# Kernel optimization log

Hardware: AMD Instinct MI355X
Metric: run time of the kernel (lower is better)

## Reference

```python
import jax, jax.numpy as jnp
import numpy as np

NUM_HEADS = 16
ROPE_BASE = 10000.0

def rotate_half(x):
    h = x.shape[-1] // 2
    return jnp.concatenate([-x[..., h:], x[..., :h]], axis=-1)

def setup_inputs() -> dict:
    key = jax.random.key(0)
    k1, k2, k3, k4 = jax.random.split(key, 4)
    B, T, H = 2, 2048, 1024
    hidden_state = jax.random.normal(k1, (B, T, H), dtype=jnp.float32)
    # right-padding mask: per-batch valid lengths
    lengths = jnp.array([2048, 1536], dtype=jnp.int32)
    attention_mask = (jnp.arange(T, dtype=jnp.int32)[None, :] < lengths[:, None]).astype(jnp.int32)
    s = 1.0 / np.sqrt(H)
    w_qkv = jax.random.normal(k2, (H, 3 * H), dtype=jnp.float32) * s
    b_qkv = jax.random.normal(k3, (3 * H,), dtype=jnp.float32) * 0.01
    w_out = jax.random.normal(k4, (H, H), dtype=jnp.float32) * s
    return {"hidden_state": hidden_state, "attention_mask": attention_mask,
            "w_qkv": w_qkv, "b_qkv": b_qkv, "w_out": w_out}

def reference(hidden_state, attention_mask, w_qkv, b_qkv, w_out):
    B, T, H = hidden_state.shape
    hd = H // NUM_HEADS
    qkv = hidden_state @ w_qkv + b_qkv                      # [B,T,3H]
    qkv = qkv.reshape(B, T, NUM_HEADS, 3 * hd).swapaxes(1, 2)  # [B,h,T,3d]
    q, k, v = qkv[..., :hd], qkv[..., hd:2 * hd], qkv[..., 2 * hd:]
    # rotary embedding (cache computed in fp32, as in torch module)
    inv_freq = 1.0 / (ROPE_BASE ** (jnp.arange(0, hd, 2, dtype=jnp.float32) / hd))
    t = jnp.arange(T, dtype=jnp.float32)
    freqs = jnp.outer(t, inv_freq)                          # [T, hd/2]
    emb = jnp.concatenate([freqs, freqs], axis=-1)          # [T, hd]
    cos = jnp.cos(emb)[None, None]                          # [1,1,T,hd]
    sin = jnp.sin(emb)[None, None]
    q = q * cos + rotate_half(q) * sin
    k = k * cos + rotate_half(k) * sin
    scale = 1.0 / jnp.sqrt(jnp.asarray(hd, dtype=q.dtype))
    scores = jnp.einsum('bhqd,bhkd->bhqk', q, k) * scale    # [B,h,T,T]
    causal = jnp.triu(jnp.ones((T, T), dtype=bool), k=1)    # True = masked (future)
    pad = (attention_mask == 0)[:, None, None, :]           # True = masked (padded key)
    mask = causal[None, None] | pad
    scores = jnp.where(mask, jnp.finfo(scores.dtype).min, scores)
    attn = jax.nn.softmax(scores, axis=-1)
    out = jnp.einsum('bhqk,bhkd->bhqd', attn, v)            # [B,h,T,d]
    out = out.swapaxes(1, 2).reshape(B, T, H)
    return out @ w_out
```

## Files before the change

### kernel.cpp

```cpp
#include <hip/hip_runtime.h>
#include <math.h>

typedef __attribute__((ext_vector_type(8))) short short8;
typedef __attribute__((ext_vector_type(4))) short short4v;
typedef __attribute__((ext_vector_type(4))) float floatx4;

#define T_SEQ 2048
#define NHEADS 16
#define HID 1024

#if __has_builtin(__builtin_amdgcn_mfma_f32_16x16x16bf16_1k)
#define MFMA16(a,b,c) __builtin_amdgcn_mfma_f32_16x16x16bf16_1k(a,b,c,0,0,0)
#elif __has_builtin(__builtin_amdgcn_mfma_f32_16x16x16_bf16)
#define MFMA16(a,b,c) __builtin_amdgcn_mfma_f32_16x16x16_bf16(a,b,c,0,0,0)
#else
#define MFMA16(a,b,c) (c)
#endif

#if __has_builtin(__builtin_amdgcn_exp2f)
#define EXP2F(x) __builtin_amdgcn_exp2f(x)
#else
#define EXP2F(x) exp2f(x)
#endif

__device__ __forceinline__ ushort f2b(float x){
  union { float f; unsigned u; } c; c.f = x;
  unsigned r = c.u + 0x7fffu + ((c.u >> 16) & 1u);
  return (ushort)(r >> 16);
}

__device__ __forceinline__ floatx4 fzero4(){
  floatx4 v; v[0]=0.f; v[1]=0.f; v[2]=0.f; v[3]=0.f; return v;
}

__device__ __forceinline__ void gl_lds16(const ushort* g, ushort* l){
  __builtin_amdgcn_global_load_lds(
      (const __attribute__((address_space(1))) void*)g,
      (__attribute__((address_space(3))) void*)l, 16, 0, 0);
}


__global__ __launch_bounds__(256) void prep(
    const float* __restrict__ hidden, const float* __restrict__ w_qkv,
    const float* __restrict__ w_out, const int* __restrict__ amask,
    ushort* __restrict__ hO, ushort* __restrict__ wqkvT, ushort* __restrict__ woutT,
    float2* __restrict__ cs, int* __restrict__ Lb)
{
  __shared__ __align__(16) char smem[32 * 33 * 4];
  int blk = blockIdx.x;
  int tid = threadIdx.x;

  if (blk < 4096){
    int i = blk * 256 + tid;
    float4 v = ((const float4*)hidden)[i];
    ushort4 o;
    o.x = f2b(v.x); o.y = f2b(v.y); o.z = f2b(v.z); o.w = f2b(v.w);
    ((ushort4*)hO)[i] = o;
  } else if (blk < 8192){
    const float* in; ushort* out; int R, C, bx, by;
    if (blk < 7168){
      int t = blk - 4096; bx = t % 96; by = t / 96;
      in = w_qkv; out = wqkvT; R = 1024; C = 3072;
    } else {
      int t = blk - 7168; bx = t & 31; by = t >> 5;
      in = w_out; out = woutT; R = 1024; C = 1024;
    }
    float (*tile)[33] = (float(*)[33])smem;
    int c0 = bx * 32, r0 = by * 32;
    int tx = tid & 31, ty = tid >> 5;
    #pragma unroll
    for (int i = 0; i < 4; i++){
      int r = ty + i * 8;
      tile[r][tx] = in[(size_t)(r0 + r) * C + c0 + tx];
    }
    __syncthreads();
    #pragma unroll
    for (int i = 0; i < 4; i++){
      int r = ty + i * 8;
      out[(size_t)(c0 + r) * R + r0 + tx] = f2b(tile[tx][r]);
    }
  } else if (blk < 8448){
    int idx = (blk - 8192) * 256 + tid;
    int t = idx >> 5, i = idx & 31;
    float invf = powf(10000.0f, -(float)i / 32.0f);
    float a = (float)t * invf;
    cs[idx] = make_float2(cosf(a), sinf(a));
  } else {
    int b = blk - 8448;
    int* red = (int*)smem;
    int s = 0;
    for (int i = tid; i < T_SEQ; i += 256) s += amask[b * T_SEQ + i];
    red[tid] = s; __syncthreads();
    for (int o = 128; o > 0; o >>= 1){
      if (tid < o) red[tid] += red[tid + o];
      __syncthreads();
    }
    if (tid == 0) Lb[b] = red[0];
  }
}


__global__ __launch_bounds__(256) void gemm_qkv(
    const ushort* __restrict__ A, const ushort* __restrict__ Bt,
    const float* __restrict__ bias,
    ushort* __restrict__ qO, ushort* __restrict__ kO, ushort* __restrict__ vT,
    const float2* __restrict__ cs)
{
  __shared__ __align__(16) ushort As[2][4096];
  __shared__ __align__(16) ushort Bs[2][4096];
  int tid = threadIdx.x;
  int bm = blockIdx.x, bn = blockIdx.y;
  int wave = tid >> 6, lane = tid & 63;
  int wm = wave >> 1, wn = wave & 1;
  int quad = lane >> 4, l15 = lane & 15;

  int srow0 = wave * 32 + (lane >> 2);
  int scol  = (lane & 3) * 8;
  const ushort* baseA = &A[(size_t)(bm * 128 + srow0) * 1024 + scol];
  const ushort* baseB = &Bt[(size_t)(bn * 128 + srow0) * 1024 + scol];

  floatx4 acc[4][4];
  for (int i = 0; i < 4; i++) for (int j = 0; j < 4; j++) acc[i][j] = fzero4();

  gl_lds16(baseA,             &As[0][wave * 1024]);
  gl_lds16(baseA + 16 * 1024, &As[0][wave * 1024 + 512]);
  gl_lds16(baseB,             &Bs[0][wave * 1024]);
  gl_lds16(baseB + 16 * 1024, &Bs[0][wave * 1024 + 512]);
  __syncthreads();

  for (int kt = 0; kt < 32; ++kt){
    int cur = kt & 1;
    if (kt < 31){
      const ushort* gA = baseA + (kt + 1) * 32;
      const ushort* gB = baseB + (kt + 1) * 32;
      gl_lds16(gA,             &As[cur ^ 1][wave * 1024]);
      gl_lds16(gA + 16 * 1024, &As[cur ^ 1][wave * 1024 + 512]);
      gl_lds16(gB,             &Bs[cur ^ 1][wave * 1024]);
      gl_lds16(gB + 16 * 1024, &Bs[cur ^ 1][wave * 1024 + 512]);
    }
    short8 af[4], bfr[4];
    #pragma unroll
    for (int i = 0; i < 4; i++) af[i]  = *(const short8*)&As[cur][(wm * 64 + i * 16 + l15) * 32 + quad * 8];
    #pragma unroll
    for (int i = 0; i < 4; i++) bfr[i] = *(const short8*)&Bs[cur][(wn * 64 + i * 16 + l15) * 32 + quad * 8];
    #pragma unroll
    for (int mt = 0; mt < 4; mt++)
      #pragma unroll
      for (int nt = 0; nt < 4; nt++)
        acc[mt][nt] = __builtin_amdgcn_mfma_f32_16x16x32_bf16(af[mt], bfr[nt], acc[mt][nt], 0, 0, 0);
    __syncthreads();
  }

  int g = bn * 2 + wn;
  int h = g / 3, comp = g - h * 3;

  if (comp == 2){
    #pragma unroll
    for (int nt = 0; nt < 4; nt++){
      int d = nt * 16 + l15;
      float bv = bias[g * 64 + d];
      #pragma unroll
      for (int mt = 0; mt < 4; mt++){
        int row = bm * 128 + wm * 64 + mt * 16 + quad * 4;
        int t = row & (T_SEQ - 1), b_ = row >> 11;
        ushort4 o;
        o.x = f2b(acc[mt][nt][0] + bv);
        o.y = f2b(acc[mt][nt][1] + bv);
        o.z = f2b(acc[mt][nt][2] + bv);
        o.w = f2b(acc[mt][nt][3] + bv);
        *(ushort4*)&vT[(size_t)((b_ * NHEADS + h) * 64 + d) * T_SEQ + t] = o;
      }
    }
  } else {
    ushort* outP = (comp == 0) ? qO : kO;
    float qs = (comp == 0) ? 0.125f * 1.44269504089f : 1.0f;
    float bv[4], bp[4];
    #pragma unroll
    for (int nt = 0; nt < 4; nt++){
      bv[nt] = bias[g * 64 + nt * 16 + l15];
      bp[nt] = bias[g * 64 + ((nt * 16 + l15) ^ 32)];
    }
    #pragma unroll
    for (int mt = 0; mt < 4; mt++)
      #pragma unroll
      for (int r = 0; r < 4; r++){
        int row = bm * 128 + wm * 64 + mt * 16 + quad * 4 + r;
        int t = row & (T_SEQ - 1), b_ = row >> 11;
        float2 c0 = cs[t * 32 + l15];
        float2 c1 = cs[t * 32 + 16 + l15];
        size_t base = (size_t)((b_ * NHEADS + h) * T_SEQ + t) * 64 + l15;
        #pragma unroll
        for (int nt = 0; nt < 4; nt++){
          float cvv = (nt & 1) ? c1.x : c0.x;
          float svv = (nt & 1) ? c1.y : c0.y;
          float sgn = (nt < 2) ? -1.0f : 1.0f;
          float val = acc[mt][nt][r] + bv[nt];
          float pv  = acc[mt][nt ^ 2][r] + bp[nt];
          outP[base + nt * 16] = f2b((val * cvv + sgn * pv * svv) * qs);
        }
      }
  }
}


__global__ __launch_bounds__(256) void attn(
    const ushort* __restrict__ qB, const ushort* __restrict__ kB,
    const ushort* __restrict__ vTB, const int* __restrict__ Lb,
    ushort* __restrict__ oB)
{
  __shared__ __align__(16) ushort SH[2][8192];
  int tid = threadIdx.x;
  int bh = blockIdx.x;
  int qt = 31 - blockIdx.y;
  int b = bh >> 4, h = bh & 15;
  int wave = tid >> 6, lane = tid & 63;
  int quad = lane >> 4, l15 = lane & 15;
  int q0 = qt * 64;
  int L = Lb[b];

  const ushort* Qb  = qB + (size_t)bh * T_SEQ * 64;
  const ushort* Kb  = kB + (size_t)bh * T_SEQ * 64;
  const ushort* VtB = vTB + (size_t)bh * 64 * T_SEQ;

  int qrow = q0 + wave * 16 + l15;
  short8 qf0 = *(const short8*)&Qb[(size_t)qrow * 64 + quad * 8];
  short8 qf1 = *(const short8*)&Qb[(size_t)qrow * 64 + 32 + quad * 8];

  int lr = lane >> 3, ch = lane & 7;
  int sw = (ch ^ lr) * 8;
  int l7 = l15 & 7;

  float l_i = 0.f;
  floatx4 oacc[4];
  #pragma unroll
  for (int nt = 0; nt < 4; nt++) oacc[nt] = fzero4();

  int lastkb = qt;
  int lkb2 = (L - 1) >> 6;
  if (lkb2 < lastkb) lastkb = lkb2;

  auto stageKV = [&](int kb, int buf){
    int k0 = kb * 64;
    const ushort* gK = &Kb[(size_t)(k0 + wave * 16 + lr) * 64 + sw];
    gl_lds16(gK,          &SH[buf][(wave * 16) * 64]);
    gl_lds16(gK + 8 * 64, &SH[buf][(wave * 16 + 8) * 64]);
    const ushort* gV = &VtB[(size_t)(wave * 16 + lr) * T_SEQ + k0 + sw];
    gl_lds16(gV,             &SH[buf][4096 + (wave * 16) * 64]);
    gl_lds16(gV + 8 * T_SEQ, &SH[buf][4096 + (wave * 16 + 8) * 64]);
  };

  stageKV(0, 0);
  __syncthreads();

  for (int kb = 0; kb <= lastkb; ++kb){
    int cur = kb & 1;
    if (kb < lastkb) stageKV(kb + 1, cur ^ 1);
    const ushort* Ks = &SH[cur][0];
    const ushort* Vt = &SH[cur][4096];
    int k0 = kb * 64;

    floatx4 sacc[4];
    #pragma unroll
    for (int e = 0; e < 4; e++){
      short8 kf0 = *(const short8*)&Ks[(e * 16 + l15) * 64 + ((quad ^ l7) * 8)];
      short8 kf1 = *(const short8*)&Ks[(e * 16 + l15) * 64 + (((quad | 4) ^ l7) * 8)];
      floatx4 z = fzero4();
      z = __builtin_amdgcn_mfma_f32_16x16x32_bf16(kf0, qf0, z, 0, 0, 0);
      z = __builtin_amdgcn_mfma_f32_16x16x32_bf16(kf1, qf1, z, 0, 0, 0);
      sacc[e] = z;
    }

    float p[4][4];
    bool needm = (kb == qt) || (k0 + 64 > L);
    if (needm){
      #pragma unroll
      for (int e = 0; e < 4; e++)
        #pragma unroll
        for (int r = 0; r < 4; r++){
          int key = k0 + e * 16 + quad * 4 + r;
          float ev = EXP2F(sacc[e][r]);
          p[e][r] = (key <= qrow && key < L) ? ev : 0.f;
        }
    } else {
      #pragma unroll
      for (int e = 0; e < 4; e++)
        #pragma unroll
        for (int r = 0; r < 4; r++) p[e][r] = EXP2F(sacc[e][r]);
    }
    float s0 = 0.f, s1 = 0.f, s2 = 0.f, s3 = 0.f;
    #pragma unroll
    for (int e = 0; e < 4; e++){
      s0 += p[e][0]; s1 += p[e][1]; s2 += p[e][2]; s3 += p[e][3];
    }
    l_i += (s0 + s1) + (s2 + s3);

    short4v pf[4];
    #pragma unroll
    for (int e = 0; e < 4; e++){
      union { unsigned u[2]; short4v v; } pk;
      pk.u[0] = (__float_as_uint(p[e][1]) & 0xffff0000u) | (__float_as_uint(p[e][0]) >> 16);
      pk.u[1] = (__float_as_uint(p[e][3]) & 0xffff0000u) | (__float_as_uint(p[e][2]) >> 16);
      pf[e] = pk.v;
    }

    #pragma unroll
    for (int nt = 0; nt < 4; nt++){
      #pragma unroll
      for (int e = 0; e < 4; e++){
        int cw = e * 2 + (quad >> 1);
        short4v vf = *(const short4v*)&Vt[(nt * 16 + l15) * 64 + ((cw ^ l7) * 8) + (quad & 1) * 4];
        oacc[nt] = MFMA16(vf, pf[e], oacc[nt]);
      }
    }
    __syncthreads();
  }

  l_i += __shfl_xor(l_i, 16);
  l_i += __shfl_xor(l_i, 32);
  float inv = 1.f / l_i;

  ushort (*Ot)[80] = (ushort(*)[80])&SH[0][0];
  #pragma unroll
  for (int nt = 0; nt < 4; nt++){
    ushort4 o;
    o.x = f2b(oacc[nt][0] * inv);
    o.y = f2b(oacc[nt][1] * inv);
    o.z = f2b(oacc[nt][2] * inv);
    o.w = f2b(oacc[nt][3] * inv);
    *(ushort4*)&Ot[wave * 16 + l15][nt * 16 + quad * 4] = o;
  }
  __syncthreads();
  int r = tid >> 2, c = (tid & 3) * 16;
  short8 o0 = *(const short8*)&Ot[r][c];
  short8 o1 = *(const short8*)&Ot[r][c + 8];
  ushort* dst = &oB[(size_t)((b * T_SEQ + q0 + r) * NHEADS + h) * 64 + c];
  *(short8*)dst = o0;
  *(short8*)(dst + 8) = o1;
}


__global__ __launch_bounds__(256) void gemm_out_k(
    const ushort* __restrict__ A, const ushort* __restrict__ Bt,
    float* __restrict__ out)
{
  __shared__ __align__(16) ushort As[2][4096];
  __shared__ __align__(16) ushort Bs[2][2048];
  int tid = threadIdx.x;
  int bm = blockIdx.x, bn = blockIdx.y;
  int wave = tid >> 6, lane = tid & 63;
  int wm = wave >> 1, wn = wave & 1;
  int quad = lane >> 4, l15 = lane & 15;

  int lr4 = lane >> 2;
  int sc  = (lane & 3) * 8;
  const ushort* baseA = &A[(size_t)(bm * 128 + wave * 32 + lr4) * 1024 + sc];
  const ushort* baseB = &Bt[(size_t)(bn * 64 + wave * 16 + lr4) * 1024 + sc];

  floatx4 acc[4][2];
  for (int i = 0; i < 4; i++) for (int j = 0; j < 2; j++) acc[i][j] = fzero4();

  gl_lds16(baseA,             &As[0][wave * 1024]);
  gl_lds16(baseA + 16 * 1024, &As[0][wave * 1024 + 512]);
  gl_lds16(baseB,             &Bs[0][wave * 512]);
  __syncthreads();

  for (int kt = 0; kt < 32; ++kt){
    int cur = kt & 1;
    if (kt < 31){
      const ushort* gA = baseA + (kt + 1) * 32;
      const ushort* gB = baseB + (kt + 1) * 32;
      gl_lds16(gA,             &As[cur ^ 1][wave * 1024]);
      gl_lds16(gA + 16 * 1024, &As[cur ^ 1][wave * 1024 + 512]);
      gl_lds16(gB,             &Bs[cur ^ 1][wave * 512]);
    }
    short8 af[4], bfr[2];
    #pragma unroll
    for (int i = 0; i < 4; i++) af[i]  = *(const short8*)&As[cur][(wm * 64 + i * 16 + l15) * 32 + quad * 8];
    #pragma unroll
    for (int j = 0; j < 2; j++) bfr[j] = *(const short8*)&Bs[cur][(wn * 32 + j * 16 + l15) * 32 + quad * 8];
    #pragma unroll
    for (int mt = 0; mt < 4; mt++)
      #pragma unroll
      for (int nt = 0; nt < 2; nt++)
        acc[mt][nt] = __builtin_amdgcn_mfma_f32_16x16x32_bf16(af[mt], bfr[nt], acc[mt][nt], 0, 0, 0);
    __syncthreads();
  }

  #pragma unroll
  for (int nt = 0; nt < 2; nt++){
    int n = bn * 64 + wn * 32 + nt * 16 + l15;
    #pragma unroll
    for (int mt = 0; mt < 4; mt++)
      #pragma unroll
      for (int r = 0; r < 4; r++){
        int row = bm * 128 + wm * 64 + mt * 16 + quad * 4 + r;
        out[(size_t)row * 1024 + n] = acc[mt][nt][r];
      }
  }
}


extern "C" void kernel_launch(void* const* d_in, const int* in_sizes, int n_in,
                              void* d_out, int out_size, void* d_ws, size_t ws_size,
                              hipStream_t stream)
{
  const float* hidden = (const float*)d_in[0];
  const int*   amask  = (const int*)d_in[1];
  const float* w_qkv  = (const float*)d_in[2];
  const float* b_qkv  = (const float*)d_in[3];
  const float* w_out  = (const float*)d_in[4];
  float* out = (float*)d_out;

  char* ws = (char*)d_ws;
  ushort* hO    = (ushort*)(ws);
  ushort* wqkvT = (ushort*)(ws + 8388608);
  ushort* woutT = (ushort*)(ws + 14680064);
  ushort* qB    = (ushort*)(ws + 16777216);
  ushort* kB    = (ushort*)(ws + 25165824);
  ushort* vT    = (ushort*)(ws + 33554432);
  float2* cs    = (float2*)(ws + 41943040);
  int*    Lb    = (int*)(ws + 42467328);

  prep<<<8450, 256, 0, stream>>>(hidden, w_qkv, w_out, amask, hO, wqkvT, woutT, cs, Lb);
  gemm_qkv<<<dim3(32, 24), 256, 0, stream>>>(hO, wqkvT, b_qkv, qB, kB, vT, cs);
  attn<<<dim3(32, 32), 256, 0, stream>>>(qB, kB, vT, Lb, hO );
  gemm_out_k<<<dim3(32, 16), 256, 0, stream>>>(hO, woutT, out);
}
```

Baseline: 179.5 us.

## Restructure QKV GEMM to 256x256 tiles with swizzled LDS and staged pipeline

The QKV projection GEMM moves from 128x128 tiles with 4 waves to 256x256 tiles with 8 waves and a K-step of 64. It XOR-swizzles the LDS layout to avoid bank conflicts and remaps block IDs so neighbouring blocks share operand tiles in cache. It also splits each K-step into four MFMA phases, interleaving global-to-LDS prefetch with barriers and s_setprio. The aim is more operand reuse per byte loaded and better overlap of loads with MFMA, at the cost of only 192 blocks and higher register and LDS use (128KB of LDS per block).

```diff
diff --git a/kernel.cpp b/kernel.cpp
--- a/kernel.cpp
+++ b/kernel.cpp
@@ -100,58 +100,133 @@
 }
 
 
-__global__ __launch_bounds__(256) void gemm_qkv(
+__global__ __launch_bounds__(512, 2) void gemm_qkv(
     const ushort* __restrict__ A, const ushort* __restrict__ Bt,
     const float* __restrict__ bias,
     ushort* __restrict__ qO, ushort* __restrict__ kO, ushort* __restrict__ vT,
     const float2* __restrict__ cs)
 {
-  __shared__ __align__(16) ushort As[2][4096];
-  __shared__ __align__(16) ushort Bs[2][4096];
+  __shared__ __align__(16) ushort As[2][16384];
+  __shared__ __align__(16) ushort Bs[2][16384];
   int tid = threadIdx.x;
-  int bm = blockIdx.x, bn = blockIdx.y;
+  int bid = blockIdx.x;
+  int swz = (bid & 7) * 24 + (bid >> 3);
+  int bm = swz / 12, bn = swz - bm * 12;
   int wave = tid >> 6, lane = tid & 63;
-  int wm = wave >> 1, wn = wave & 1;
-  int quad = lane >> 4, l15 = lane & 15;
-
-  int srow0 = wave * 32 + (lane >> 2);
-  int scol  = (lane & 3) * 8;
-  const ushort* baseA = &A[(size_t)(bm * 128 + srow0) * 1024 + scol];
-  const ushort* baseB = &Bt[(size_t)(bn * 128 + srow0) * 1024 + scol];
-
-  floatx4 acc[4][4];
-  for (int i = 0; i < 4; i++) for (int j = 0; j < 4; j++) acc[i][j] = fzero4();
-
-  gl_lds16(baseA,             &As[0][wave * 1024]);
-  gl_lds16(baseA + 16 * 1024, &As[0][wave * 1024 + 512]);
-  gl_lds16(baseB,             &Bs[0][wave * 1024]);
-  gl_lds16(baseB + 16 * 1024, &Bs[0][wave * 1024 + 512]);
-  __syncthreads();
-
-  for (int kt = 0; kt < 32; ++kt){
+  int wm = wave >> 2, wn = wave & 3;
+  int quad = lane >> 4, l15 = lane & 15, l7 = lane & 7;
+
+  int srow = tid >> 3, sslot = tid & 7;
+  const ushort* gA = A  + (size_t)(bm * 256 + srow) * 1024 + ((sslot ^ (srow & 7)) << 3);
+  const ushort* gB = Bt + (size_t)(bn * 256 + srow) * 1024 + ((sslot ^ (srow & 7)) << 3);
+
+  auto stageA = [&](int buf, int kt){
+    #pragma unroll
+    for (int i = 0; i < 4; i++)
+      gl_lds16(gA + (size_t)i * 64 * 1024 + kt * 64, &As[buf][i * 4096 + wave * 512]);
+  };
+  auto stageB = [&](int buf, int kt){
+    #pragma unroll
+    for (int i = 0; i < 4; i++)
+      gl_lds16(gB + (size_t)i * 64 * 1024 + kt * 64, &Bs[buf][i * 4096 + wave * 512]);
+  };
+
+  int s0 = ((quad)     ^ l7) << 3;
+  int s1 = ((quad + 4) ^ l7) << 3;
+
+  floatx4 acc[8][4];
+  #pragma unroll
+  for (int i = 0; i < 8; i++)
+    #pragma unroll
+    for (int j = 0; j < 4; j++) acc[i][j] = fzero4();
+
+  stageA(0, 0); stageB(0, 0);
+  asm volatile("s_waitcnt vmcnt(0)" ::: "memory");
+  __builtin_amdgcn_s_barrier();
+
+  short8 af[4][2], bfr[4][2];
+
+  for (int kt = 0; kt < 16; ++kt){
     int cur = kt & 1;
-    if (kt < 31){
-      const ushort* gA = baseA + (kt + 1) * 32;
-      const ushort* gB = baseB + (kt + 1) * 32;
-      gl_lds16(gA,             &As[cur ^ 1][wave * 1024]);
-      gl_lds16(gA + 16 * 1024, &As[cur ^ 1][wave * 1024 + 512]);
-      gl_lds16(gB,             &Bs[cur ^ 1][wave * 1024]);
-      gl_lds16(gB + 16 * 1024, &Bs[cur ^ 1][wave * 1024 + 512]);
-    }
-    short8 af[4], bfr[4];
-    #pragma unroll
-    for (int i = 0; i < 4; i++) af[i]  = *(const short8*)&As[cur][(wm * 64 + i * 16 + l15) * 32 + quad * 8];
-    #pragma unroll
-    for (int i = 0; i < 4; i++) bfr[i] = *(const short8*)&Bs[cur][(wn * 64 + i * 16 + l15) * 32 + quad * 8];
+    const ushort* Ac = &As[cur][0];
+    const ushort* Bc = &Bs[cur][0];
+
+    #pragma unroll
+    for (int mt = 0; mt < 4; mt++){
+      int ro = (wm * 128 + mt * 16 + l15) * 64;
+      af[mt][0] = *(const short8*)&Ac[ro + s0];
+      af[mt][1] = *(const short8*)&Ac[ro + s1];
+    }
+    #pragma unroll
+    for (int nt = 0; nt < 2; nt++){
+      int ro = (wn * 64 + nt * 16 + l15) * 64;
+      bfr[nt][0] = *(const short8*)&Bc[ro + s0];
+      bfr[nt][1] = *(const short8*)&Bc[ro + s1];
+    }
+    if (kt < 15) stageA(cur ^ 1, kt + 1);
+    __builtin_amdgcn_s_barrier();
+    __builtin_amdgcn_s_setprio(1);
     #pragma unroll
     for (int mt = 0; mt < 4; mt++)
       #pragma unroll
-      for (int nt = 0; nt < 4; nt++)
-        acc[mt][nt] = __builtin_amdgcn_mfma_f32_16x16x32_bf16(af[mt], bfr[nt], acc[mt][nt], 0, 0, 0);
-    __syncthreads();
-  }
-
-  int g = bn * 2 + wn;
+      for (int nt = 0; nt < 2; nt++){
+        acc[mt][nt] = __builtin_amdgcn_mfma_f32_16x16x32_bf16(af[mt][0], bfr[nt][0], acc[mt][nt], 0, 0, 0);
+        acc[mt][nt] = __builtin_amdgcn_mfma_f32_16x16x32_bf16(af[mt][1], bfr[nt][1], acc[mt][nt], 0, 0, 0);
+      }
+    __builtin_amdgcn_s_setprio(0);
+    __builtin_amdgcn_s_barrier();
+
+    #pragma unroll
+    for (int nt = 2; nt < 4; nt++){
+      int ro = (wn * 64 + nt * 16 + l15) * 64;
+      bfr[nt][0] = *(const short8*)&Bc[ro + s0];
+      bfr[nt][1] = *(const short8*)&Bc[ro + s1];
+    }
+    if (kt < 15) stageB(cur ^ 1, kt + 1);
+    __builtin_amdgcn_s_barrier();
+    __builtin_amdgcn_s_setprio(1);
+    #pragma unroll
+    for (int mt = 0; mt < 4; mt++)
+      #pragma unroll
+      for (int nt = 2; nt < 4; nt++){
+        acc[mt][nt] = __builtin_amdgcn_mfma_f32_16x16x32_bf16(af[mt][0], bfr[nt][0], acc[mt][nt], 0, 0, 0);
+        acc[mt][nt] = __builtin_amdgcn_mfma_f32_16x16x32_bf16(af[mt][1], bfr[nt][1], acc[mt][nt], 0, 0, 0);
+      }
+    __builtin_amdgcn_s_setprio(0);
+    __builtin_amdgcn_s_barrier();
+
+    #pragma unroll
+    for (int mt = 0; mt < 4; mt++){
+      int ro = (wm * 128 + 64 + mt * 16 + l15) * 64;
+      af[mt][0] = *(const short8*)&Ac[ro + s0];
+      af[mt][1] = *(const short8*)&Ac[ro + s1];
+    }
+    __builtin_amdgcn_s_barrier();
+    __builtin_amdgcn_s_setprio(1);
+    #pragma unroll
+    for (int mt = 0; mt < 4; mt++)
+      #pragma unroll
+      for (int nt = 0; nt < 2; nt++){
+        acc[4 + mt][nt] = __builtin_amdgcn_mfma_f32_16x16x32_bf16(af[mt][0], bfr[nt][0], acc[4 + mt][nt], 0, 0, 0);
+        acc[4 + mt][nt] = __builtin_amdgcn_mfma_f32_16x16x32_bf16(af[mt][1], bfr[nt][1], acc[4 + mt][nt], 0, 0, 0);
+      }
+    __builtin_amdgcn_s_setprio(0);
+    __builtin_amdgcn_s_barrier();
+
+    __builtin_amdgcn_s_setprio(1);
+    #pragma unroll
+    for (int mt = 0; mt < 4; mt++)
+      #pragma unroll
+      for (int nt = 2; nt < 4; nt++){
+        acc[4 + mt][nt] = __builtin_amdgcn_mfma_f32_16x16x32_bf16(af[mt][0], bfr[nt][0], acc[4 + mt][nt], 0, 0, 0);
+        acc[4 + mt][nt] = __builtin_amdgcn_mfma_f32_16x16x32_bf16(af[mt][1], bfr[nt][1], acc[4 + mt][nt], 0, 0, 0);
+      }
+    __builtin_amdgcn_s_setprio(0);
+    if (kt < 15) asm volatile("s_waitcnt vmcnt(0)" ::: "memory");
+    __builtin_amdgcn_s_barrier();
+  }
+
+  int g = bn * 4 + wn;
   int h = g / 3, comp = g - h * 3;
 
   if (comp == 2){
@@ -160,8 +235,8 @@
       int d = nt * 16 + l15;
       float bv = bias[g * 64 + d];
       #pragma unroll
-      for (int mt = 0; mt < 4; mt++){
-        int row = bm * 128 + wm * 64 + mt * 16 + quad * 4;
+      for (int mt = 0; mt < 8; mt++){
+        int row = bm * 256 + wm * 128 + mt * 16 + quad * 4;
         int t = row & (T_SEQ - 1), b_ = row >> 11;
         ushort4 o;
         o.x = f2b(acc[mt][nt][0] + bv);
@@ -181,10 +256,10 @@
       bp[nt] = bias[g * 64 + ((nt * 16 + l15) ^ 32)];
     }
     #pragma unroll
-    for (int mt = 0; mt < 4; mt++)
+    for (int mt = 0; mt < 8; mt++)
       #pragma unroll
       for (int r = 0; r < 4; r++){
-        int row = bm * 128 + wm * 64 + mt * 16 + quad * 4 + r;
+        int row = bm * 256 + wm * 128 + mt * 16 + quad * 4 + r;
         int t = row & (T_SEQ - 1), b_ = row >> 11;
         float2 c0 = cs[t * 32 + l15];
         float2 c1 = cs[t * 32 + 16 + l15];
@@ -422,7 +497,7 @@
   int*    Lb    = (int*)(ws + 42467328);
 
   prep<<<8450, 256, 0, stream>>>(hidden, w_qkv, w_out, amask, hO, wqkvT, woutT, cs, Lb);
-  gemm_qkv<<<dim3(32, 24), 256, 0, stream>>>(hO, wqkvT, b_qkv, qB, kB, vT, cs);
+  gemm_qkv<<<dim3(192), 512, 0, stream>>>(hO, wqkvT, b_qkv, qB, kB, vT, cs);
   attn<<<dim3(32, 32), 256, 0, stream>>>(qB, kB, vT, Lb, hO );
   gemm_out_k<<<dim3(32, 16), 256, 0, stream>>>(hO, woutT, out);
 }
```

Result: no change. 179.3 us (-0.2%).

## Enlarge QKV GEMM tile to 256x256 with 8 waves and swizzled LDS

Applied to the files above, without the earlier changes.

The QKV projection GEMM now uses 256x256 output tiles computed by 8 waves (512 threads), with a 64-wide K step split into two halves. It adds an XOR swizzle on LDS columns to avoid bank conflicts, a block-index remap for L2 locality, explicit vmcnt waits with raw barriers, and interleaves the next tile's loads with MFMA groups under raised wave priority. The goal is more reuse per loaded byte and better overlap of global-to-LDS traffic with matrix math. In exchange it uses far more LDS and registers per block, and launches only 192 blocks, which may underfill the GPU.

```diff
diff --git a/kernel.cpp b/kernel.cpp
--- a/kernel.cpp
+++ b/kernel.cpp
@@ -100,58 +100,91 @@
 }
 
 
-__global__ __launch_bounds__(256) void gemm_qkv(
+__global__ __launch_bounds__(512, 2) void gemm_qkv(
     const ushort* __restrict__ A, const ushort* __restrict__ Bt,
     const float* __restrict__ bias,
     ushort* __restrict__ qO, ushort* __restrict__ kO, ushort* __restrict__ vT,
     const float2* __restrict__ cs)
 {
-  __shared__ __align__(16) ushort As[2][4096];
-  __shared__ __align__(16) ushort Bs[2][4096];
+  __shared__ __align__(16) ushort As[2][16384];
+  __shared__ __align__(16) ushort Bs[2][16384];
   int tid = threadIdx.x;
-  int bm = blockIdx.x, bn = blockIdx.y;
+  int bid = blockIdx.x;
+  int swz = (bid & 7) * 24 + (bid >> 3);
+  int bm = swz / 12, bn = swz - bm * 12;
   int wave = tid >> 6, lane = tid & 63;
-  int wm = wave >> 1, wn = wave & 1;
+  int wm = wave >> 2, wn = wave & 3;
   int quad = lane >> 4, l15 = lane & 15;
 
-  int srow0 = wave * 32 + (lane >> 2);
-  int scol  = (lane & 3) * 8;
-  const ushort* baseA = &A[(size_t)(bm * 128 + srow0) * 1024 + scol];
-  const ushort* baseB = &Bt[(size_t)(bn * 128 + srow0) * 1024 + scol];
-
-  floatx4 acc[4][4];
-  for (int i = 0; i < 4; i++) for (int j = 0; j < 4; j++) acc[i][j] = fzero4();
-
-  gl_lds16(baseA,             &As[0][wave * 1024]);
-  gl_lds16(baseA + 16 * 1024, &As[0][wave * 1024 + 512]);
-  gl_lds16(baseB,             &Bs[0][wave * 1024]);
-  gl_lds16(baseB + 16 * 1024, &Bs[0][wave * 1024 + 512]);
-  __syncthreads();
-
-  for (int kt = 0; kt < 32; ++kt){
-    int cur = kt & 1;
-    if (kt < 31){
-      const ushort* gA = baseA + (kt + 1) * 32;
-      const ushort* gB = baseB + (kt + 1) * 32;
-      gl_lds16(gA,             &As[cur ^ 1][wave * 1024]);
-      gl_lds16(gA + 16 * 1024, &As[cur ^ 1][wave * 1024 + 512]);
-      gl_lds16(gB,             &Bs[cur ^ 1][wave * 1024]);
-      gl_lds16(gB + 16 * 1024, &Bs[cur ^ 1][wave * 1024 + 512]);
-    }
-    short8 af[4], bfr[4];
-    #pragma unroll
-    for (int i = 0; i < 4; i++) af[i]  = *(const short8*)&As[cur][(wm * 64 + i * 16 + l15) * 32 + quad * 8];
-    #pragma unroll
-    for (int i = 0; i < 4; i++) bfr[i] = *(const short8*)&Bs[cur][(wn * 64 + i * 16 + l15) * 32 + quad * 8];
-    #pragma unroll
-    for (int mt = 0; mt < 4; mt++)
-      #pragma unroll
-      for (int nt = 0; nt < 4; nt++)
-        acc[mt][nt] = __builtin_amdgcn_mfma_f32_16x16x32_bf16(af[mt], bfr[nt], acc[mt][nt], 0, 0, 0);
-    __syncthreads();
-  }
-
-  int g = bn * 2 + wn;
+  int srow = tid >> 2;
+  int sg = (lane & 3) ^ ((lane >> 3) & 3);
+  const ushort* gA = A  + (size_t)(bm * 256 + srow) * 1024 + sg * 8;
+  const ushort* gB = Bt + (size_t)(bn * 256 + srow) * 1024 + sg * 8;
+
+  auto stageU = [&](const ushort* g, ushort* Lbase, int kh, int kt2){
+    #pragma unroll
+    for (int i = 0; i < 2; i++)
+      gl_lds16(g + (size_t)(i * 128) * 1024 + kt2 * 64 + kh * 32,
+               Lbase + kh * 8192 + (i * 128 + wave * 16) * 32);
+  };
+
+  int sA = (quad ^ ((l15 >> 1) & 3)) * 8;
+
+  floatx4 acc[8][4];
+  #pragma unroll
+  for (int i = 0; i < 8; i++)
+    #pragma unroll
+    for (int j = 0; j < 4; j++) acc[i][j] = fzero4();
+
+  stageU(gA, &As[0][0], 0, 0);
+  stageU(gB, &Bs[0][0], 0, 0);
+  stageU(gA, &As[0][0], 1, 0);
+  stageU(gB, &Bs[0][0], 1, 0);
+
+  for (int kt = 0; kt < 16; ++kt){
+    int cur = kt & 1, nxt = cur ^ 1;
+    const ushort* Ac = &As[cur][0];
+    const ushort* Bc = &Bs[cur][0];
+
+    #pragma unroll
+    for (int kh = 0; kh < 2; kh++){
+      if (kh == 0 || kt < 15) asm volatile("s_waitcnt vmcnt(4)" ::: "memory");
+      else                    asm volatile("s_waitcnt vmcnt(0)" ::: "memory");
+      __builtin_amdgcn_s_barrier();
+
+      short8 af[8], bfr[4];
+      #pragma unroll
+      for (int mt = 0; mt < 8; mt++)
+        af[mt] = *(const short8*)&Ac[kh * 8192 + (wm * 128 + mt * 16 + l15) * 32 + sA];
+      #pragma unroll
+      for (int nt = 0; nt < 2; nt++)
+        bfr[nt] = *(const short8*)&Bc[kh * 8192 + (wn * 64 + nt * 16 + l15) * 32 + sA];
+      if (kt < 15) stageU(gA, &As[nxt][0], kh, kt + 1);
+
+      __builtin_amdgcn_s_setprio(1);
+      #pragma unroll
+      for (int mt = 0; mt < 8; mt++)
+        #pragma unroll
+        for (int nt = 0; nt < 2; nt++)
+          acc[mt][nt] = __builtin_amdgcn_mfma_f32_16x16x32_bf16(af[mt], bfr[nt], acc[mt][nt], 0, 0, 0);
+      __builtin_amdgcn_s_setprio(0);
+
+      #pragma unroll
+      for (int nt = 2; nt < 4; nt++)
+        bfr[nt] = *(const short8*)&Bc[kh * 8192 + (wn * 64 + nt * 16 + l15) * 32 + sA];
+      if (kt < 15) stageU(gB, &Bs[nxt][0], kh, kt + 1);
+
+      __builtin_amdgcn_s_setprio(1);
+      #pragma unroll
+      for (int mt = 0; mt < 8; mt++)
+        #pragma unroll
+        for (int nt = 2; nt < 4; nt++)
+          acc[mt][nt] = __builtin_amdgcn_mfma_f32_16x16x32_bf16(af[mt], bfr[nt], acc[mt][nt], 0, 0, 0);
+      __builtin_amdgcn_s_setprio(0);
+    }
+  }
+
+  int g = bn * 4 + wn;
   int h = g / 3, comp = g - h * 3;
 
   if (comp == 2){
@@ -160,8 +193,8 @@
       int d = nt * 16 + l15;
       float bv = bias[g * 64 + d];
       #pragma unroll
-      for (int mt = 0; mt < 4; mt++){
-        int row = bm * 128 + wm * 64 + mt * 16 + quad * 4;
+      for (int mt = 0; mt < 8; mt++){
+        int row = bm * 256 + wm * 128 + mt * 16 + quad * 4;
         int t = row & (T_SEQ - 1), b_ = row >> 11;
         ushort4 o;
         o.x = f2b(acc[mt][nt][0] + bv);
@@ -181,10 +214,10 @@
       bp[nt] = bias[g * 64 + ((nt * 16 + l15) ^ 32)];
     }
     #pragma unroll
-    for (int mt = 0; mt < 4; mt++)
+    for (int mt = 0; mt < 8; mt++)
       #pragma unroll
       for (int r = 0; r < 4; r++){
-        int row = bm * 128 + wm * 64 + mt * 16 + quad * 4 + r;
+        int row = bm * 256 + wm * 128 + mt * 16 + quad * 4 + r;
         int t = row & (T_SEQ - 1), b_ = row >> 11;
         float2 c0 = cs[t * 32 + l15];
         float2 c1 = cs[t * 32 + 16 + l15];
@@ -422,7 +455,7 @@
   int*    Lb    = (int*)(ws + 42467328);
 
   prep<<<8450, 256, 0, stream>>>(hidden, w_qkv, w_out, amask, hO, wqkvT, woutT, cs, Lb);
-  gemm_qkv<<<dim3(32, 24), 256, 0, stream>>>(hO, wqkvT, b_qkv, qB, kB, vT, cs);
+  gemm_qkv<<<dim3(192), 512, 0, stream>>>(hO, wqkvT, b_qkv, qB, kB, vT, cs);
   attn<<<dim3(32, 32), 256, 0, stream>>>(qB, kB, vT, Lb, hO );
   gemm_out_k<<<dim3(32, 16), 256, 0, stream>>>(hO, woutT, out);
 }
```

New measurement: 175.4 us. 1.02x faster.
